# Performance work log

Hardware: AMD Instinct MI355X
Metric: run time of the kernel (lower is better)

Reference implementation:

```python
import jax, jax.numpy as jnp
import numpy as np

D_MODEL = 512
NUM_HEADS = 8
HEAD_DIM = D_MODEL // NUM_HEADS
CTX = 20
EPS = 1e-5


def _layernorm(x, w, b):
    mu = jnp.mean(x, axis=-1, keepdims=True)
    var = jnp.var(x, axis=-1, keepdims=True)
    return (x - mu) * jax.lax.rsqrt(var + EPS) * w + b


def setup_inputs() -> dict:
    key = jax.random.key(0)
    ks = jax.random.split(key, 12)
    B, T = 4096, CTX
    s_attn = 1.0 / np.sqrt(D_MODEL)
    s_ffn1 = 1.0 / np.sqrt(D_MODEL)
    s_ffn2 = 1.0 / np.sqrt(4 * D_MODEL)
    return {
        "x": jax.random.normal(ks[0], (B, T, D_MODEL), dtype=jnp.float32),
        "ln1_w": jnp.ones((D_MODEL,), jnp.float32),
        "ln1_b": jnp.zeros((D_MODEL,), jnp.float32),
        # per-head projections stacked: [H, D, head_dim]
        "Wq": jax.random.normal(ks[1], (NUM_HEADS, D_MODEL, HEAD_DIM), dtype=jnp.float32) * s_attn,
        "Wk": jax.random.normal(ks[2], (NUM_HEADS, D_MODEL, HEAD_DIM), dtype=jnp.float32) * s_attn,
        "Wv": jax.random.normal(ks[3], (NUM_HEADS, D_MODEL, HEAD_DIM), dtype=jnp.float32) * s_attn,
        "Wo": jax.random.normal(ks[4], (D_MODEL, D_MODEL), dtype=jnp.float32) * s_attn,
        "Wo_b": jnp.zeros((D_MODEL,), jnp.float32),
        "ln2_w": jnp.ones((D_MODEL,), jnp.float32),
        "ln2_b": jnp.zeros((D_MODEL,), jnp.float32),
        "W1": jax.random.normal(ks[5], (D_MODEL, 4 * D_MODEL), dtype=jnp.float32) * s_ffn1,
        "b1": jnp.zeros((4 * D_MODEL,), jnp.float32),
        "W2": jax.random.normal(ks[6], (4 * D_MODEL, D_MODEL), dtype=jnp.float32) * s_ffn2,
        "b2": jnp.zeros((D_MODEL,), jnp.float32),
    }


def reference(x, ln1_w, ln1_b, Wq, Wk, Wv, Wo, Wo_b, ln2_w, ln2_b, W1, b1, W2, b2):
    B, T, D = x.shape
    # --- multi-head attention (dropout = identity, eval mode) ---
    h = _layernorm(x, ln1_w, ln1_b)
    # [B,T,D] x [H,D,hd] -> [B,H,T,hd]
    q = jnp.einsum('btd,hde->bhte', h, Wq)
    k = jnp.einsum('btd,hde->bhte', h, Wk)
    v = jnp.einsum('btd,hde->bhte', h, Wv)
    scores = jnp.einsum('bhte,bhse->bhts', q, k) / np.sqrt(HEAD_DIM)
    mask = jnp.tril(jnp.ones((T, T), dtype=bool))
    scores = jnp.where(mask, scores, -jnp.inf)
    attn = jax.nn.softmax(scores, axis=-1)
    ctx = jnp.einsum('bhts,bhse->bhte', attn, v)  # [B,H,T,hd]
    # concat heads along last dim (head order matches torch cat)
    ctx = jnp.transpose(ctx, (0, 2, 1, 3)).reshape(B, T, D)
    attn_out = ctx @ Wo.T + Wo_b
    x = x + attn_out
    # --- FFN ---
    h2 = _layernorm(x, ln2_w, ln2_b)
    ff = jax.nn.relu(h2 @ W1 + b1) @ W2 + b2
    return x + ff
```

## Files before the change

### kernel.cpp

```cpp
#include <hip/hip_runtime.h>

typedef __attribute__((ext_vector_type(8))) short short8;
typedef __attribute__((ext_vector_type(4))) float float4v;

__device__ __forceinline__ float b2f(ushort u) {
  union { uint i; float f; } c; c.i = ((uint)u) << 16; return c.f;
}
__device__ __forceinline__ ushort f2b(float f) {
  union { float f; uint i; } c; c.f = f;
  return (ushort)((c.i + 0x7fffu + ((c.i >> 16) & 1u)) >> 16);
}
__device__ __forceinline__ float ldin(const void* p, size_t i, int f32) {
  return f32 ? ((const float*)p)[i] : b2f(((const ushort*)p)[i]);
}
__device__ __forceinline__ void load_lds16(const ushort* g, ushort* l) {
  __builtin_amdgcn_global_load_lds((__attribute__((address_space(1))) const void*)g,
                                   (__attribute__((address_space(3))) void*)l, 16, 0, 0);
}

__global__ void detect(const void* w1, int* flag) {
  const uint u = *(const uint*)w1;
  *flag = (u == 0x3F800000u) ? 1 : 0;
}

__global__ __launch_bounds__(256) void gemm_bt(
    const ushort* __restrict__ A, const ushort* __restrict__ B,
    void* C, const ushort* __restrict__ bias, const void* res,
    const int* resflagp, const int* outflagp,
    int M, int N, int K, int relu)
{
  __shared__ ushort lA[128 * 64];
  __shared__ ushort lB[128 * 64];
  const int w = threadIdx.x >> 6;
  const int l = threadIdx.x & 63;
  const int mBase = blockIdx.y * 128;
  const int nBase = blockIdx.x * 128;
  const int wr = w >> 1, wc = w & 1;
  const int lrow = l >> 3;
  const int lcol = (l & 7) * 8;

  const float4v vzero = {0.f, 0.f, 0.f, 0.f};
  float4v acc[4][4];
#pragma unroll
  for (int i = 0; i < 4; ++i)
#pragma unroll
    for (int j = 0; j < 4; ++j) acc[i][j] = vzero;

  for (int k0 = 0; k0 < K; k0 += 64) {
#pragma unroll
    for (int i = 0; i < 4; ++i) {
      const int s = w + i * 4;
      load_lds16(A + (size_t)(mBase + s * 8 + lrow) * K + k0 + lcol, &lA[s * 512]);
      load_lds16(B + (size_t)(nBase + s * 8 + lrow) * K + k0 + lcol, &lB[s * 512]);
    }
    __syncthreads();
#pragma unroll
    for (int kk = 0; kk < 64; kk += 32) {
      const int kof = kk + (l >> 4) * 8;
      short8 af[4], bf[4];
#pragma unroll
      for (int i = 0; i < 4; ++i)
        af[i] = *(const short8*)&lA[(wr * 64 + i * 16 + (l & 15)) * 64 + kof];
#pragma unroll
      for (int j = 0; j < 4; ++j)
        bf[j] = *(const short8*)&lB[(wc * 64 + j * 16 + (l & 15)) * 64 + kof];
#pragma unroll
      for (int i = 0; i < 4; ++i)
#pragma unroll
        for (int j = 0; j < 4; ++j)
          acc[i][j] = __builtin_amdgcn_mfma_f32_16x16x32_bf16(af[i], bf[j], acc[i][j], 0, 0, 0);
    }
    __syncthreads();
  }

  const int rf32 = (res && resflagp) ? *resflagp : 0;
  const int of32 = outflagp ? *outflagp : 0;
  const int r0 = mBase + wr * 64 + (l >> 4) * 4;
  const int c0 = nBase + wc * 64 + (l & 15);
#pragma unroll
  for (int j = 0; j < 4; ++j) {
    const int col = c0 + j * 16;
    const float bv = bias ? b2f(bias[col]) : 0.f;
#pragma unroll
    for (int i = 0; i < 4; ++i) {
#pragma unroll
      for (int r = 0; r < 4; ++r) {
        const size_t off = (size_t)(r0 + i * 16 + r) * N + col;
        float v = acc[i][j][r] + bv;
        if (res) v += rf32 ? ((const float*)res)[off] : b2f(((const ushort*)res)[off]);
        if (relu) v = fmaxf(v, 0.f);
        if (of32) ((float*)C)[off] = v;
        else      ((ushort*)C)[off] = f2b(v);
      }
    }
  }
}

__global__ __launch_bounds__(256) void lnorm(const void* __restrict__ x,
                                             const ushort* __restrict__ gw,
                                             const ushort* __restrict__ gb,
                                             ushort* __restrict__ out,
                                             const int* flagp)
{
  const int f32 = flagp ? *flagp : 0;
  const int tok = blockIdx.x * 4 + (threadIdx.x >> 6);
  const int l = threadIdx.x & 63;
  const size_t base = (size_t)tok * 512 + l * 8;
  float v[8];
  if (f32) {
    const float4* p = (const float4*)((const float*)x + base);
    float4 a = p[0], b = p[1];
    v[0]=a.x; v[1]=a.y; v[2]=a.z; v[3]=a.w; v[4]=b.x; v[5]=b.y; v[6]=b.z; v[7]=b.w;
  } else {
    uint4 u = *(const uint4*)((const ushort*)x + base);
    uint uu[4] = {u.x, u.y, u.z, u.w};
#pragma unroll
    for (int i = 0; i < 4; ++i) {
      v[2*i]   = b2f((ushort)(uu[i] & 0xffffu));
      v[2*i+1] = b2f((ushort)(uu[i] >> 16));
    }
  }
  float s = 0.f, ss = 0.f;
#pragma unroll
  for (int i = 0; i < 8; ++i) { s += v[i]; ss += v[i] * v[i]; }
  for (int off = 32; off > 0; off >>= 1) {
    s  += __shfl_xor(s, off, 64);
    ss += __shfl_xor(ss, off, 64);
  }
  const float mean = s * (1.f / 512.f);
  const float var  = ss * (1.f / 512.f) - mean * mean;
  const float inv  = rsqrtf(var + 1e-5f);
  uint4 uwv = *(const uint4*)(gw + l * 8);
  uint4 ubv = *(const uint4*)(gb + l * 8);
  uint uws[4] = {uwv.x, uwv.y, uwv.z, uwv.w};
  uint ubs[4] = {ubv.x, ubv.y, ubv.z, ubv.w};
  uint ro[4];
#pragma unroll
  for (int i = 0; i < 4; ++i) {
    float w0 = b2f((ushort)(uws[i] & 0xffffu)), w1 = b2f((ushort)(uws[i] >> 16));
    float b0 = b2f((ushort)(ubs[i] & 0xffffu)), b1 = b2f((ushort)(ubs[i] >> 16));
    float y0 = (v[2*i]   - mean) * inv * w0 + b0;
    float y1 = (v[2*i+1] - mean) * inv * w1 + b1;
    ro[i] = (uint)f2b(y0) | ((uint)f2b(y1) << 16);
  }
  uint4 o; o.x = ro[0]; o.y = ro[1]; o.z = ro[2]; o.w = ro[3];
  *(uint4*)(out + base) = o;
}

__global__ __launch_bounds__(128) void attn(const ushort* __restrict__ QKV,
                                            ushort* __restrict__ ctx)
{
  __shared__ float sq[2][20][65];
  __shared__ float sk[2][20][65];
  __shared__ float sv[2][20][65];
  __shared__ float sp[2][20][33];
  const int w = threadIdx.x >> 6;
  const int l = threadIdx.x & 63;
  const int idx = blockIdx.x * 2 + w;
  const int b = idx >> 3, h = idx & 7;
  const ushort* base = QKV + (size_t)b * 20 * 1536 + h * 64;
#pragma unroll
  for (int tp = 0; tp < 10; ++tp) {
    const int t = tp * 2 + (l >> 5);
    const int e2 = (l & 31) * 2;
    const uint uq = *(const uint*)&base[t * 1536 + e2];
    const uint uk = *(const uint*)&base[t * 1536 + 512 + e2];
    const uint uv = *(const uint*)&base[t * 1536 + 1024 + e2];
    sq[w][t][e2] = b2f((ushort)(uq & 0xffffu)); sq[w][t][e2+1] = b2f((ushort)(uq >> 16));
    sk[w][t][e2] = b2f((ushort)(uk & 0xffffu)); sk[w][t][e2+1] = b2f((ushort)(uk >> 16));
    sv[w][t][e2] = b2f((ushort)(uv & 0xffffu)); sv[w][t][e2+1] = b2f((ushort)(uv >> 16));
  }
  __syncthreads();
  for (int tp = 0; tp < 10; ++tp) {
    const int t = tp * 2 + (l >> 5);
    const int s = l & 31;
    const int sr = (s < 20) ? s : 19;
    float d = 0.f;
#pragma unroll 8
    for (int e = 0; e < 64; ++e) d += sq[w][t][e] * sk[w][sr][e];
    const bool valid = (s <= t) && (s < 20);
    float sc = valid ? d * 0.125f : -1e30f;
    float m = sc;
    for (int off = 16; off > 0; off >>= 1) m = fmaxf(m, __shfl_xor(m, off, 32));
    float p = valid ? __expf(sc - m) : 0.f;
    float sum = p;
    for (int off = 16; off > 0; off >>= 1) sum += __shfl_xor(sum, off, 32);
    if (s < 20) sp[w][t][s] = p / sum;
  }
  __syncthreads();
  ushort* cbase = ctx + (size_t)b * 20 * 512 + h * 64 + l;
  for (int t = 0; t < 20; ++t) {
    float o = 0.f;
    for (int s = 0; s <= t; ++s) o += sp[w][t][s] * sv[w][s][l];
    cbase[t * 512] = f2b(o);
  }
}

__global__ __launch_bounds__(256) void pack_w(
    const void* Wq, const void* Wk, const void* Wv, const void* Wo,
    const void* W1, const void* W2,
    const void* ln1w, const void* ln1b, const void* ln2w, const void* ln2b,
    const void* Wob, const void* b1v, const void* b2v,
    const int* flagp,
    ushort* __restrict__ Wqkv_t, ushort* __restrict__ W1_t,
    ushort* __restrict__ W2_t, ushort* __restrict__ Wo_c,
    ushort* __restrict__ smalls)
{
  const int f32 = *flagp;
  const int i = blockIdx.x * 256 + threadIdx.x;
  if (i < 786432) {
    const int m = i / 262144;
    const int r = i - m * 262144;
    const void* src = (m == 0) ? Wq : ((m == 1) ? Wk : Wv);
    const int hh = r >> 15, d = (r >> 6) & 511, e = r & 63;
    Wqkv_t[(size_t)(m * 512 + hh * 64 + e) * 512 + d] = f2b(ldin(src, r, f32));
  } else if (i < 1835008) {
    const int r = i - 786432;
    const int d = r >> 11, f = r & 2047;
    W1_t[(size_t)f * 512 + d] = f2b(ldin(W1, r, f32));
  } else if (i < 2883584) {
    const int r = i - 1835008;
    const int f = r >> 9, o = r & 511;
    W2_t[(size_t)o * 2048 + f] = f2b(ldin(W2, r, f32));
  } else if (i < 3145728) {
    const int r = i - 2883584;
    Wo_c[r] = f2b(ldin(Wo, r, f32));
  } else {
    const int r = i - 3145728;
    const void* src; int idx;
    if      (r < 512)  { src = ln1w; idx = r; }
    else if (r < 1024) { src = ln1b; idx = r - 512; }
    else if (r < 1536) { src = ln2w; idx = r - 1024; }
    else if (r < 2048) { src = ln2b; idx = r - 1536; }
    else if (r < 2560) { src = Wob;  idx = r - 2048; }
    else if (r < 3072) { src = b2v;  idx = r - 2560; }
    else               { src = b1v;  idx = r - 3072; }
    smalls[r] = f2b(ldin(src, idx, f32));
  }
}

extern "C" void kernel_launch(void* const* d_in, const int* in_sizes, int n_in,
                              void* d_out, int out_size, void* d_ws, size_t ws_size,
                              hipStream_t stream) {
  char* ws = (char*)d_ws;
  int*    flag   = (int*)ws;
  ushort* Wqkv_t = (ushort*)(ws + 4096);
  ushort* W1_t   = (ushort*)(ws + 1576960ull);
  ushort* W2_t   = (ushort*)(ws + 3674112ull);
  ushort* Wo_c   = (ushort*)(ws + 5771264ull);
  ushort* smalls = (ushort*)(ws + 6295552ull);
  ushort* QKV    = (ushort*)(ws + 8388608ull);
  ushort* ff1    = QKV;
  ushort* ctxb   = (ushort*)(ws + 260046848ull);
  ushort* h      = (ushort*)(ws + 343932928ull);
  ushort* x2     = (ushort*)(ws + 427819008ull);

  detect<<<1, 1, 0, stream>>>(d_in[1], flag);
  pack_w<<<12308, 256, 0, stream>>>(d_in[3], d_in[4], d_in[5], d_in[6],
                                    d_in[10], d_in[12],
                                    d_in[1], d_in[2], d_in[8], d_in[9],
                                    d_in[7], d_in[11], d_in[13],
                                    flag, Wqkv_t, W1_t, W2_t, Wo_c, smalls);
  lnorm<<<20480, 256, 0, stream>>>(d_in[0], smalls + 0, smalls + 512, h, flag);
  gemm_bt<<<dim3(12, 640), 256, 0, stream>>>(h, Wqkv_t, QKV, nullptr, nullptr,
                                             nullptr, nullptr, 81920, 1536, 512, 0);
  attn<<<16384, 128, 0, stream>>>(QKV, ctxb);
  gemm_bt<<<dim3(4, 640), 256, 0, stream>>>(ctxb, Wo_c, x2, smalls + 2048, d_in[0],
                                            flag, nullptr, 81920, 512, 512, 0);
  lnorm<<<20480, 256, 0, stream>>>(x2, smalls + 1024, smalls + 1536, h, nullptr);
  gemm_bt<<<dim3(16, 640), 256, 0, stream>>>(h, W1_t, ff1, smalls + 3072, nullptr,
                                             nullptr, nullptr, 81920, 2048, 512, 1);
  gemm_bt<<<dim3(4, 640), 256, 0, stream>>>(ff1, W2_t, d_out, smalls + 2560, x2,
                                            nullptr, flag, 81920, 512, 2048, 0);
}
```

Before: 1.946 ms.

## Swizzle GEMM LDS tiles, remap block order, and cache bf16 residual copy

XOR-swizzles the 16-byte column chunks of the GEMM shared-memory tiles so that MFMA fragment reads avoid bank conflicts. Converts the 2D grid to a 1D grid that groups eight M-bands at a time so neighbouring blocks share B tiles in L2. The first layernorm also writes a bf16 copy of x, which the Wo GEMM reads as its residual in place of the fp32 input. That halves the residual read bandwidth but adds a write pass and extra workspace, and the residual is rounded to bf16.

```diff
diff --git a/kernel.cpp b/kernel.cpp
--- a/kernel.cpp
+++ b/kernel.cpp
@@ -27,17 +27,21 @@
     const ushort* __restrict__ A, const ushort* __restrict__ B,
     void* C, const ushort* __restrict__ bias, const void* res,
     const int* resflagp, const int* outflagp,
-    int M, int N, int K, int relu)
+    int M, int N, int K, int relu, int nb)
 {
   __shared__ ushort lA[128 * 64];
   __shared__ ushort lB[128 * 64];
   const int w = threadIdx.x >> 6;
   const int l = threadIdx.x & 63;
-  const int mBase = blockIdx.y * 128;
-  const int nBase = blockIdx.x * 128;
+  const int bid = blockIdx.x;
+  const int low3 = bid & 7, rest = bid >> 3;
+  const int n_idx = rest % nb;
+  const int band  = ((rest / nb) << 3) | low3;
+  const int mBase = band * 128;
+  const int nBase = n_idx * 128;
   const int wr = w >> 1, wc = w & 1;
   const int lrow = l >> 3;
-  const int lcol = (l & 7) * 8;
+  const int lcolsw = (((l & 7) ^ lrow) * 8);
 
   const float4v vzero = {0.f, 0.f, 0.f, 0.f};
   float4v acc[4][4];
@@ -50,20 +54,21 @@
 #pragma unroll
     for (int i = 0; i < 4; ++i) {
       const int s = w + i * 4;
-      load_lds16(A + (size_t)(mBase + s * 8 + lrow) * K + k0 + lcol, &lA[s * 512]);
-      load_lds16(B + (size_t)(nBase + s * 8 + lrow) * K + k0 + lcol, &lB[s * 512]);
+      load_lds16(A + (size_t)(mBase + s * 8 + lrow) * K + k0 + lcolsw, &lA[s * 512]);
+      load_lds16(B + (size_t)(nBase + s * 8 + lrow) * K + k0 + lcolsw, &lB[s * 512]);
     }
     __syncthreads();
 #pragma unroll
     for (int kk = 0; kk < 64; kk += 32) {
-      const int kof = kk + (l >> 4) * 8;
+      const int ch = (kk >> 3) + (l >> 4);
+      const int csw = (ch ^ (l & 7)) * 8;
       short8 af[4], bf[4];
 #pragma unroll
       for (int i = 0; i < 4; ++i)
-        af[i] = *(const short8*)&lA[(wr * 64 + i * 16 + (l & 15)) * 64 + kof];
+        af[i] = *(const short8*)&lA[(wr * 64 + i * 16 + (l & 15)) * 64 + csw];
 #pragma unroll
       for (int j = 0; j < 4; ++j)
-        bf[j] = *(const short8*)&lB[(wc * 64 + j * 16 + (l & 15)) * 64 + kof];
+        bf[j] = *(const short8*)&lB[(wc * 64 + j * 16 + (l & 15)) * 64 + csw];
 #pragma unroll
       for (int i = 0; i < 4; ++i)
 #pragma unroll
@@ -100,6 +105,7 @@
                                              const ushort* __restrict__ gw,
                                              const ushort* __restrict__ gb,
                                              ushort* __restrict__ out,
+                                             ushort* __restrict__ xcopy,
                                              const int* flagp)
 {
   const int f32 = flagp ? *flagp : 0;
@@ -119,6 +125,14 @@
       v[2*i]   = b2f((ushort)(uu[i] & 0xffffu));
       v[2*i+1] = b2f((ushort)(uu[i] >> 16));
     }
+  }
+  if (xcopy) {
+    uint xo[4];
+#pragma unroll
+    for (int i = 0; i < 4; ++i)
+      xo[i] = (uint)f2b(v[2*i]) | ((uint)f2b(v[2*i+1]) << 16);
+    uint4 xv; xv.x = xo[0]; xv.y = xo[1]; xv.z = xo[2]; xv.w = xo[3];
+    *(uint4*)(xcopy + base) = xv;
   }
   float s = 0.f, ss = 0.f;
 #pragma unroll
@@ -254,6 +268,8 @@
   ushort* ctxb   = (ushort*)(ws + 260046848ull);
   ushort* h      = (ushort*)(ws + 343932928ull);
   ushort* x2     = (ushort*)(ws + 427819008ull);
+  ushort* xbf    = (ushort*)(ws + 511705088ull);
+  const bool have_xbf = ws_size >= 595591168ull;
 
   detect<<<1, 1, 0, stream>>>(d_in[1], flag);
   pack_w<<<12308, 256, 0, stream>>>(d_in[3], d_in[4], d_in[5], d_in[6],
@@ -261,15 +277,18 @@
                                     d_in[1], d_in[2], d_in[8], d_in[9],
                                     d_in[7], d_in[11], d_in[13],
                                     flag, Wqkv_t, W1_t, W2_t, Wo_c, smalls);
-  lnorm<<<20480, 256, 0, stream>>>(d_in[0], smalls + 0, smalls + 512, h, flag);
-  gemm_bt<<<dim3(12, 640), 256, 0, stream>>>(h, Wqkv_t, QKV, nullptr, nullptr,
-                                             nullptr, nullptr, 81920, 1536, 512, 0);
+  lnorm<<<20480, 256, 0, stream>>>(d_in[0], smalls + 0, smalls + 512, h,
+                                   have_xbf ? xbf : nullptr, flag);
+  gemm_bt<<<12 * 640, 256, 0, stream>>>(h, Wqkv_t, QKV, nullptr, nullptr,
+                                        nullptr, nullptr, 81920, 1536, 512, 0, 12);
   attn<<<16384, 128, 0, stream>>>(QKV, ctxb);
-  gemm_bt<<<dim3(4, 640), 256, 0, stream>>>(ctxb, Wo_c, x2, smalls + 2048, d_in[0],
-                                            flag, nullptr, 81920, 512, 512, 0);
-  lnorm<<<20480, 256, 0, stream>>>(x2, smalls + 1024, smalls + 1536, h, nullptr);
-  gemm_bt<<<dim3(16, 640), 256, 0, stream>>>(h, W1_t, ff1, smalls + 3072, nullptr,
-                                             nullptr, nullptr, 81920, 2048, 512, 1);
-  gemm_bt<<<dim3(4, 640), 256, 0, stream>>>(ff1, W2_t, d_out, smalls + 2560, x2,
-                                            nullptr, flag, 81920, 512, 2048, 0);
-}
+  gemm_bt<<<4 * 640, 256, 0, stream>>>(ctxb, Wo_c, x2, smalls + 2048,
+                                       have_xbf ? (const void*)xbf : (const void*)d_in[0],
+                                       have_xbf ? nullptr : flag, nullptr,
+                                       81920, 512, 512, 0, 4);
+  lnorm<<<20480, 256, 0, stream>>>(x2, smalls + 1024, smalls + 1536, h, nullptr, nullptr);
+  gemm_bt<<<16 * 640, 256, 0, stream>>>(h, W1_t, ff1, smalls + 3072, nullptr,
+                                        nullptr, nullptr, 81920, 2048, 512, 1, 16);
+  gemm_bt<<<4 * 640, 256, 0, stream>>>(ff1, W2_t, d_out, smalls + 2560, x2,
+                                       nullptr, flag, 81920, 512, 2048, 0, 4);
+}
```

New measurement: 1.716 ms. 11.8% less time.
